# Kernel optimization log

Hardware: AMD Instinct MI355X
Metric: run time of the kernel (lower is better)

Reference implementation:

```python
import jax, jax.numpy as jnp
import numpy as np

H = 3  # heads
NEG_SLOPE = 0.2


def gat_conv(x, edge_index, W, a_src, a_dst, bias):
    # PyG GATConv: add self loops, per-head linear, edge attention, segment softmax over dst.
    N = x.shape[0]
    C = a_src.shape[1]
    loop = jnp.arange(N)
    src = jnp.concatenate([edge_index[0], loop])
    dst = jnp.concatenate([edge_index[1], loop])
    h = (x @ W).reshape(N, H, C)                      # [N,H,C]
    s_src = jnp.sum(h * a_src, axis=-1)               # [N,H]
    s_dst = jnp.sum(h * a_dst, axis=-1)               # [N,H]
    e = jax.nn.leaky_relu(s_src[src] + s_dst[dst], NEG_SLOPE)  # [E,H]
    m = jax.ops.segment_max(e, dst, num_segments=N)   # every node has a self loop -> finite
    e = jnp.exp(e - m[dst])
    denom = jax.ops.segment_sum(e, dst, num_segments=N)
    alpha = e / (denom[dst] + 1e-16)                  # [E,H]
    out = jax.ops.segment_sum(alpha[:, :, None] * h[src], dst, num_segments=N)  # [N,H,C]
    return out.reshape(N, H * C) + bias


def mlp(x, w1, b1, w2, b2):
    return jax.nn.gelu(x @ w1 + b1, approximate=False) @ w2 + b2


def glorot(k, shape):
    fan_in, fan_out = shape[-2], shape[-1]
    lim = np.sqrt(6.0 / (fan_in + fan_out))
    return jax.random.uniform(k, shape, jnp.float32, -lim, lim)


def setup_inputs() -> dict:
    key = jax.random.key(0)
    ks = jax.random.split(key, 24)
    N, E, F, C, HID = 50000, 800000, 256, 64, 128
    inp = {
        "x_st": jax.random.normal(ks[0], (N, F), jnp.float32),
        "edge_index_st": jax.random.randint(ks[1], (2, E), 0, N, jnp.int32),
        "x_sc": jax.random.normal(ks[2], (N, F), jnp.float32),
        "edge_index_sc": jax.random.randint(ks[3], (2, E), 0, N, jnp.int32),
    }
    for i, tag in enumerate(["st", "sc"]):
        o = 4 + i * 10
        inp[f"w_gat_{tag}"] = glorot(ks[o], (F, H * C))
        inp[f"a_src_{tag}"] = glorot(ks[o + 1], (H, C)) * 0.1
        inp[f"a_dst_{tag}"] = glorot(ks[o + 2], (H, C)) * 0.1
        inp[f"b_gat_{tag}"] = jnp.zeros((H * C,), jnp.float32)
        inp[f"w1_{tag}"] = glorot(ks[o + 3], (H * C, HID))
        inp[f"b1_{tag}"] = jnp.zeros((HID,), jnp.float32)
        inp[f"w2_{tag}"] = glorot(ks[o + 4], (HID, 1))
        inp[f"b2_{tag}"] = jnp.zeros((1,), jnp.float32)
    return inp


def reference(x_st, edge_index_st, x_sc, edge_index_sc,
              w_gat_st, a_src_st, a_dst_st, b_gat_st, w1_st, b1_st, w2_st, b2_st,
              w_gat_sc, a_src_sc, a_dst_sc, b_gat_sc, w1_sc, b1_sc, w2_sc, b2_sc):
    weight = 0.5
    h_st = jax.nn.elu(gat_conv(x_st, edge_index_st, w_gat_st, a_src_st, a_dst_st, b_gat_st))
    beta_st = mlp(h_st, w1_st, b1_st, w2_st, b2_st) / 100.0   # [N,1]
    z_st = x_st.T @ beta_st                                   # [F,1]
    h_sc = jax.nn.elu(gat_conv(x_sc, edge_index_sc, w_gat_sc, a_src_sc, a_dst_sc, b_gat_sc))
    beta_sc = mlp(h_sc, w1_sc, b1_sc, w2_sc, b2_sc) / 100.0
    z_sc = x_sc.T @ beta_sc
    out = jax.nn.sigmoid(z_sc + weight * z_st)
    return (out, beta_st, beta_sc)
```

## Files before the change

### kernel.cpp

```cpp
#include <hip/hip_runtime.h>
#include <math.h>

#define HEADS 3
#define CDIM 64
#define FDIM 256
#define HC 192
#define HIDDIM 128
#define NEG 0.2f

#define SCAN_BLK 256
#define SCAN_ELEMS 1024

#define ASTR2 40
#define BSTR 264
#define BSTRB 200

typedef __attribute__((ext_vector_type(8))) short short8;
typedef __attribute__((ext_vector_type(4))) float f32x4;

__device__ __forceinline__ void atomicMaxF(float* addr, float val) {
    if (val >= 0.f) atomicMax((int*)addr, __float_as_int(val));
    else            atomicMin((unsigned int*)addr, __float_as_uint(val));
}

__device__ __forceinline__ unsigned short f2bf(float f) {
    unsigned int u = __float_as_uint(f);
    u = (u + 0x7FFFu + ((u >> 16) & 1u)) >> 16;
    return (unsigned short)u;
}
__device__ __forceinline__ float bf2f(unsigned short u) {
    return __uint_as_float((unsigned int)u << 16);
}
__device__ __forceinline__ float leaky(float s) { return s >= 0.f ? s : NEG * s; }

__device__ __forceinline__ int xcd_swizzle(int orig, int nwg) {
    int q = nwg >> 3, r = nwg & 7;
    int xcd = orig & 7, idx = orig >> 3;
    return (xcd < r ? xcd * (q + 1) : r * (q + 1) + (xcd - r) * q) + idx;
}

__global__ __launch_bounds__(256) void setup(const float* __restrict__ wg_st,
                                             const float* __restrict__ wg_sc,
                                             const float* __restrict__ w1_st,
                                             const float* __restrict__ w1_sc,
                                             unsigned short* __restrict__ o0,
                                             unsigned short* __restrict__ o1,
                                             unsigned short* __restrict__ o2,
                                             unsigned short* __restrict__ o3,
                                             int* __restrict__ zero_base, int zero_ints) {
    int which = blockIdx.y;
    if (which == 4) {
        for (int i = blockIdx.x * 256 + threadIdx.x; i < zero_ints; i += gridDim.x * 256)
            zero_base[i] = 0;
        return;
    }
    const float* src = which == 0 ? wg_st : which == 1 ? wg_sc : which == 2 ? w1_st : w1_sc;
    unsigned short* dst = which == 0 ? o0 : which == 1 ? o1 : which == 2 ? o2 : o3;
    int K  = which < 2 ? FDIM : HC;
    int Nn = which < 2 ? HC : HIDDIM;
    int total = K * Nn;
    for (int idx = blockIdx.x * 256 + threadIdx.x; idx < total; idx += gridDim.x * 256) {
        int n = idx / K, k = idx - n * K;
        dst[idx] = f2bf(src[(size_t)k * Nn + n]);
    }
}

__global__ __launch_bounds__(256) void gemm_attn(const float* __restrict__ x_st,
                                                 const float* __restrict__ x_sc,
                                                 const unsigned short* __restrict__ wgT_st,
                                                 const unsigned short* __restrict__ wgT_sc,
                                                 const float* __restrict__ as_st,
                                                 const float* __restrict__ ad_st,
                                                 const float* __restrict__ as_sc,
                                                 const float* __restrict__ ad_sc,
                                                 unsigned short* __restrict__ h_bf,
                                                 float* __restrict__ ssrc,
                                                 float* __restrict__ sdst,
                                                 int M, int nrow) {
    __shared__ unsigned short As[128 * ASTR2];
    __shared__ unsigned short Bs[64 * BSTR];
    const int nwg = nrow * HEADS * 2;
    const int wgid = xcd_swizzle(blockIdx.x, nwg);
    const int tag = wgid / (nrow * HEADS);
    const int rem = wgid - tag * (nrow * HEADS);
    const int rt = rem / HEADS;
    const int head = rem - rt * HEADS;
    const float* A = tag ? x_sc : x_st;
    const unsigned short* BT = tag ? wgT_sc : wgT_st;
    const float* a_src = tag ? as_sc : as_st;
    const float* a_dst = tag ? ad_sc : ad_st;
    const int row0 = rt * 128, col0 = head * 64;
    const int tid = threadIdx.x;
    const int wv = tid >> 6, l = tid & 63;
    const int lr = l & 15, lg = l >> 4, lk = lg * 8;
    {
        int c = tid >> 2, q = tid & 3;
        const unsigned short* bp = BT + (size_t)(col0 + c) * FDIM;
        #pragma unroll
        for (int kk = q * 8; kk < FDIM; kk += 32)
            *(short8*)(Bs + c * BSTR + kk) = *(const short8*)(bp + kk);
    }
    const int arow = tid >> 1, aseg = tid & 1;
    const int gr = row0 + arow;
    f32x4 acc[2][4] = {};
    for (int ks = 0; ks < FDIM / 32; ++ks) {
        int k0 = ks * 32;
        short8 av1 = {0,0,0,0,0,0,0,0}, av2 = {0,0,0,0,0,0,0,0};
        if (gr < M) {
            const float* p = A + (size_t)gr * FDIM + k0 + aseg * 16;
            float4 x0 = *(const float4*)p;
            float4 x1 = *(const float4*)(p + 4);
            float4 x2 = *(const float4*)(p + 8);
            float4 x3 = *(const float4*)(p + 12);
            av1[0] = (short)f2bf(x0.x); av1[1] = (short)f2bf(x0.y);
            av1[2] = (short)f2bf(x0.z); av1[3] = (short)f2bf(x0.w);
            av1[4] = (short)f2bf(x1.x); av1[5] = (short)f2bf(x1.y);
            av1[6] = (short)f2bf(x1.z); av1[7] = (short)f2bf(x1.w);
            av2[0] = (short)f2bf(x2.x); av2[1] = (short)f2bf(x2.y);
            av2[2] = (short)f2bf(x2.z); av2[3] = (short)f2bf(x2.w);
            av2[4] = (short)f2bf(x3.x); av2[5] = (short)f2bf(x3.y);
            av2[6] = (short)f2bf(x3.z); av2[7] = (short)f2bf(x3.w);
        }
        *(short8*)(As + arow * ASTR2 + aseg * 16) = av1;
        *(short8*)(As + arow * ASTR2 + aseg * 16 + 8) = av2;
        __syncthreads();
        #pragma unroll
        for (int m = 0; m < 2; ++m) {
            short8 af = *(const short8*)(As + (wv * 32 + m * 16 + lr) * ASTR2 + lk);
            #pragma unroll
            for (int nb = 0; nb < 4; ++nb) {
                short8 bfm = *(const short8*)(Bs + (nb * 16 + lr) * BSTR + k0 + lk);
                acc[m][nb] = __builtin_amdgcn_mfma_f32_16x16x32_bf16(af, bfm, acc[m][nb], 0, 0, 0);
            }
        }
        __syncthreads();
    }
    const size_t tagbase = (size_t)tag * M;
    #pragma unroll
    for (int m = 0; m < 2; ++m)
        #pragma unroll
        for (int nb = 0; nb < 4; ++nb)
            #pragma unroll
            for (int r = 0; r < 4; ++r) {
                int grow = row0 + wv * 32 + m * 16 + lg * 4 + r;
                if (grow < M)
                    h_bf[(tagbase + grow) * HC + col0 + nb * 16 + lr] = f2bf(acc[m][nb][r]);
            }
    float avs[4], avd[4];
    #pragma unroll
    for (int nb = 0; nb < 4; ++nb) {
        avs[nb] = a_src[col0 + nb * 16 + lr];
        avd[nb] = a_dst[col0 + nb * 16 + lr];
    }
    #pragma unroll
    for (int m = 0; m < 2; ++m)
        #pragma unroll
        for (int r = 0; r < 4; ++r) {
            float ds = acc[m][0][r] * avs[0] + acc[m][1][r] * avs[1]
                     + acc[m][2][r] * avs[2] + acc[m][3][r] * avs[3];
            float dd = acc[m][0][r] * avd[0] + acc[m][1][r] * avd[1]
                     + acc[m][2][r] * avd[2] + acc[m][3][r] * avd[3];
            #pragma unroll
            for (int off = 8; off; off >>= 1) {
                ds += __shfl_down(ds, off);
                dd += __shfl_down(dd, off);
            }
            int grow = row0 + wv * 32 + m * 16 + lg * 4 + r;
            if (lr == 0 && grow < M) {
                ssrc[(tagbase + grow) * 3 + head] = ds;
                sdst[(tagbase + grow) * 3 + head] = dd;
            }
        }
}

__global__ __launch_bounds__(256) void prep(const int* __restrict__ ei_st,
                                            const int* __restrict__ ei_sc,
                                            int* __restrict__ deg,
                                            const float* __restrict__ ssrc,
                                            const float* __restrict__ sdst,
                                            float* __restrict__ gmax,
                                            int N, int E, int Etot) {
    if (blockIdx.y < 2) {
        int e = blockIdx.x * 256 + threadIdx.x;
        if (e >= Etot) return;
        const int* ei = blockIdx.y ? ei_sc : ei_st;
        int dst = (e < E) ? ei[E + e] : (e - E);
        atomicAdd(&deg[blockIdx.y * N + dst], 1);
        return;
    }
    if (blockIdx.x >= 32) return;
    __shared__ float red[4][12];
    float v[12];
    #pragma unroll
    for (int j = 0; j < 12; ++j) v[j] = -1e30f;
    const int stride = 32 * 256;
    for (int n = blockIdx.x * 256 + threadIdx.x; n < 2 * N; n += stride) {
        float s0 = ssrc[n * 3], s1 = ssrc[n * 3 + 1], s2 = ssrc[n * 3 + 2];
        float d0 = sdst[n * 3], d1 = sdst[n * 3 + 1], d2 = sdst[n * 3 + 2];
        if (n < N) {
            v[0] = fmaxf(v[0], s0); v[1] = fmaxf(v[1], s1); v[2] = fmaxf(v[2], s2);
            v[3] = fmaxf(v[3], d0); v[4] = fmaxf(v[4], d1); v[5] = fmaxf(v[5], d2);
        } else {
            v[6] = fmaxf(v[6], s0); v[7] = fmaxf(v[7], s1); v[8] = fmaxf(v[8], s2);
            v[9] = fmaxf(v[9], d0); v[10] = fmaxf(v[10], d1); v[11] = fmaxf(v[11], d2);
        }
    }
    #pragma unroll
    for (int j = 0; j < 12; ++j)
        #pragma unroll
        for (int off = 32; off; off >>= 1)
            v[j] = fmaxf(v[j], __shfl_down(v[j], off));
    int wave = threadIdx.x >> 6, lane = threadIdx.x & 63;
    if (lane == 0) {
        #pragma unroll
        for (int j = 0; j < 12; ++j) red[wave][j] = v[j];
    }
    __syncthreads();
    if (threadIdx.x < 12) {
        float m = fmaxf(fmaxf(red[0][threadIdx.x], red[1][threadIdx.x]),
                        fmaxf(red[2][threadIdx.x], red[3][threadIdx.x]));
        atomicMaxF(&gmax[threadIdx.x], m);
    }
}

__global__ __launch_bounds__(SCAN_BLK) void scan1(const int* __restrict__ deg,
                                                  int* __restrict__ row_ptr,
                                                  int* __restrict__ bsums, int N2) {
    __shared__ int sm[SCAN_BLK];
    int tid = threadIdx.x;
    int base = blockIdx.x * SCAN_ELEMS + tid * 4;
    int v[4];
    #pragma unroll
    for (int j = 0; j < 4; ++j) v[j] = (base + j < N2) ? deg[base + j] : 0;
    int tsum = v[0] + v[1] + v[2] + v[3];
    sm[tid] = tsum;
    __syncthreads();
    for (int off = 1; off < SCAN_BLK; off <<= 1) {
        int y = (tid >= off) ? sm[tid - off] : 0;
        __syncthreads();
        sm[tid] += y;
        __syncthreads();
    }
    int run = sm[tid] - tsum;
    #pragma unroll
    for (int j = 0; j < 4; ++j) {
        if (base + j < N2) row_ptr[base + j] = run;
        run += v[j];
    }
    if (tid == SCAN_BLK - 1) bsums[blockIdx.x] = sm[SCAN_BLK - 1];
}

__global__ __launch_bounds__(SCAN_BLK) void scan2(int* __restrict__ bsums, int nb) {
    __shared__ int sm[SCAN_BLK];
    int tid = threadIdx.x;
    int v = (tid < nb) ? bsums[tid] : 0;
    sm[tid] = v;
    __syncthreads();
    for (int off = 1; off < SCAN_BLK; off <<= 1) {
        int y = (tid >= off) ? sm[tid - off] : 0;
        __syncthreads();
        sm[tid] += y;
        __syncthreads();
    }
    if (tid < nb) bsums[tid] = sm[tid] - v;
}

__global__ __launch_bounds__(256) void scatter_p2(const int* __restrict__ ei_st,
                                                  const int* __restrict__ ei_sc,
                                                  const float* __restrict__ s_src_all,
                                                  const float* __restrict__ s_dst_all,
                                                  const float* __restrict__ gmax,
                                                  const int* __restrict__ row_ptr,
                                                  const int* __restrict__ bsums,
                                                  int* __restrict__ cursor,
                                                  f32x4* __restrict__ csr_data,
                                                  int N, int E, int Etot) {
    int e = blockIdx.x * blockDim.x + threadIdx.x;
    if (e >= Etot) return;
    const int tag = blockIdx.y;
    const int* ei = tag ? ei_sc : ei_st;
    const float* s_src = s_src_all + (size_t)tag * N * 3;
    const float* s_dst = s_dst_all + (size_t)tag * N * 3;
    const float* gm = gmax + tag * 6;
    int src, dst;
    if (e < E) { src = ei[e]; dst = ei[E + e]; } else { src = dst = e - E; }
    float M0 = leaky(gm[0] + gm[3]);
    float M1 = leaky(gm[1] + gm[4]);
    float M2 = leaky(gm[2] + gm[5]);
    float p0 = __expf(leaky(s_src[src * 3 + 0] + s_dst[dst * 3 + 0]) - M0);
    float p1 = __expf(leaky(s_src[src * 3 + 1] + s_dst[dst * 3 + 1]) - M1);
    float p2 = __expf(leaky(s_src[src * 3 + 2] + s_dst[dst * 3 + 2]) - M2);
    int g = tag * N + dst;
    int pos = row_ptr[g] + bsums[g >> 10] + atomicAdd(&cursor[g], 1);
    f32x4 val = {__int_as_float(tag * N + src), p0, p1, p2};
    csr_data[pos] = val;
}

__global__ __launch_bounds__(256) void csr_agg2(const int* __restrict__ row_ptr,
                                                const int* __restrict__ bsums,
                                                const int* __restrict__ deg,
                                                const f32x4* __restrict__ csr_data,
                                                const unsigned short* __restrict__ Hall,
                                                const float* __restrict__ bias_st,
                                                const float* __restrict__ bias_sc,
                                                unsigned short* __restrict__ og, int N) {
    int gid = blockIdx.x * blockDim.x + threadIdx.x;
    int node = gid >> 6, lane = gid & 63;
    if (node >= 2 * N) return;
    const float* bias = (node >= N) ? bias_sc : bias_st;
    int start = row_ptr[node] + bsums[node >> 10];
    int cnt = deg[node];
    float acc0 = 0.f, acc1 = 0.f, acc2 = 0.f;
    float d0 = 0.f, d1 = 0.f, d2 = 0.f;
    int i = 0;
    for (; i + 3 < cnt; i += 4) {
        f32x4 v0 = csr_data[start + i];
        f32x4 v1 = csr_data[start + i + 1];
        f32x4 v2 = csr_data[start + i + 2];
        f32x4 v3 = csr_data[start + i + 3];
        const unsigned short* r0 =
            Hall + (size_t)__builtin_amdgcn_readfirstlane(__float_as_int(v0[0])) * HC + lane;
        const unsigned short* r1 =
            Hall + (size_t)__builtin_amdgcn_readfirstlane(__float_as_int(v1[0])) * HC + lane;
        const unsigned short* r2 =
            Hall + (size_t)__builtin_amdgcn_readfirstlane(__float_as_int(v2[0])) * HC + lane;
        const unsigned short* r3 =
            Hall + (size_t)__builtin_amdgcn_readfirstlane(__float_as_int(v3[0])) * HC + lane;
        float h00 = bf2f(r0[0]), h01 = bf2f(r0[64]), h02 = bf2f(r0[128]);
        float h10 = bf2f(r1[0]), h11 = bf2f(r1[64]), h12 = bf2f(r1[128]);
        float h20 = bf2f(r2[0]), h21 = bf2f(r2[64]), h22 = bf2f(r2[128]);
        float h30 = bf2f(r3[0]), h31 = bf2f(r3[64]), h32 = bf2f(r3[128]);
        acc0 = fmaf(v0[1], h00, acc0); acc1 = fmaf(v0[2], h01, acc1); acc2 = fmaf(v0[3], h02, acc2);
        acc0 = fmaf(v1[1], h10, acc0); acc1 = fmaf(v1[2], h11, acc1); acc2 = fmaf(v1[3], h12, acc2);
        acc0 = fmaf(v2[1], h20, acc0); acc1 = fmaf(v2[2], h21, acc1); acc2 = fmaf(v2[3], h22, acc2);
        acc0 = fmaf(v3[1], h30, acc0); acc1 = fmaf(v3[2], h31, acc1); acc2 = fmaf(v3[3], h32, acc2);
        d0 += (v0[1] + v1[1]) + (v2[1] + v3[1]);
        d1 += (v0[2] + v1[2]) + (v2[2] + v3[2]);
        d2 += (v0[3] + v1[3]) + (v2[3] + v3[3]);
    }
    for (; i < cnt; ++i) {
        f32x4 v0 = csr_data[start + i];
        const unsigned short* r0 =
            Hall + (size_t)__builtin_amdgcn_readfirstlane(__float_as_int(v0[0])) * HC + lane;
        acc0 = fmaf(v0[1], bf2f(r0[0]),   acc0);
        acc1 = fmaf(v0[2], bf2f(r0[64]),  acc1);
        acc2 = fmaf(v0[3], bf2f(r0[128]), acc2);
        d0 += v0[1]; d1 += v0[2]; d2 += v0[3];
    }
    float o0 = acc0 / (d0 + 1e-16f) + bias[lane];
    float o1 = acc1 / (d1 + 1e-16f) + bias[64 + lane];
    float o2 = acc2 / (d2 + 1e-16f) + bias[128 + lane];
    o0 = o0 > 0.f ? o0 : expm1f(o0);
    o1 = o1 > 0.f ? o1 : expm1f(o1);
    o2 = o2 > 0.f ? o2 : expm1f(o2);
    unsigned short* orow = og + (size_t)node * HC + lane;
    orow[0] = f2bf(o0); orow[64] = f2bf(o1); orow[128] = f2bf(o2);
}

__global__ __launch_bounds__(256) void gemm_beta(const unsigned short* __restrict__ og_bf,
                                                 const unsigned short* __restrict__ w1T_st,
                                                 const unsigned short* __restrict__ w1T_sc,
                                                 const float* __restrict__ b1_st,
                                                 const float* __restrict__ w2_st,
                                                 const float* __restrict__ b2_st,
                                                 const float* __restrict__ b1_sc,
                                                 const float* __restrict__ w2_sc,
                                                 const float* __restrict__ b2_sc,
                                                 float* __restrict__ beta_out,
                                                 int M, int nrow) {
    __shared__ unsigned short As[128 * ASTR2];
    __shared__ unsigned short Bs[128 * BSTRB];
    const int nwg = nrow * 2;
    const int wgid = xcd_swizzle(blockIdx.x, nwg);
    const int tag = wgid / nrow;
    const int rt = wgid - tag * nrow;
    const unsigned short* A = og_bf + (size_t)tag * M * HC;
    const unsigned short* BT = tag ? w1T_sc : w1T_st;
    const float* b1 = tag ? b1_sc : b1_st;
    const float* w2 = tag ? w2_sc : w2_st;
    const float b2v = (tag ? b2_sc : b2_st)[0];
    const int row0 = rt * 128;
    const int tid = threadIdx.x;
    const int wv = tid >> 6, l = tid & 63;
    const int lr = l & 15, lg = l >> 4, lk = lg * 8;
    {
        int c = tid >> 1, half = tid & 1;
        const unsigned short* bp = BT + (size_t)c * HC;
        #pragma unroll
        for (int j = 0; j < 12; ++j) {
            int kk = half * 96 + j * 8;
            *(short8*)(Bs + c * BSTRB + kk) = *(const short8*)(bp + kk);
        }
    }
    const int arow = tid >> 1, aseg = tid & 1;
    const int gr = row0 + arow;
    f32x4 acc[2][8] = {};
    for (int ks = 0; ks < HC / 32; ++ks) {
        int k0 = ks * 32;
        short8 av1 = {0,0,0,0,0,0,0,0}, av2 = {0,0,0,0,0,0,0,0};
        if (gr < M) {
            const unsigned short* p = A + (size_t)gr * HC + k0 + aseg * 16;
            av1 = *(const short8*)p;
            av2 = *(const short8*)(p + 8);
        }
        *(short8*)(As + arow * ASTR2 + aseg * 16) = av1;
        *(short8*)(As + arow * ASTR2 + aseg * 16 + 8) = av2;
        __syncthreads();
        #pragma unroll
        for (int m = 0; m < 2; ++m) {
            short8 af = *(const short8*)(As + (wv * 32 + m * 16 + lr) * ASTR2 + lk);
            #pragma unroll
            for (int nb = 0; nb < 8; ++nb) {
                short8 bfm = *(const short8*)(Bs + (nb * 16 + lr) * BSTRB + k0 + lk);
                acc[m][nb] = __builtin_amdgcn_mfma_f32_16x16x32_bf16(af, bfm, acc[m][nb], 0, 0, 0);
            }
        }
        __syncthreads();
    }
    float b1v[8], w2v[8];
    #pragma unroll
    for (int nb = 0; nb < 8; ++nb) {
        b1v[nb] = b1[nb * 16 + lr];
        w2v[nb] = w2[nb * 16 + lr];
    }
    #pragma unroll
    for (int m = 0; m < 2; ++m)
        #pragma unroll
        for (int r = 0; r < 4; ++r) {
            float p = 0.f;
            #pragma unroll
            for (int nb = 0; nb < 8; ++nb) {
                float vx = acc[m][nb][r] + b1v[nb];
                float g = 0.5f * vx * (1.f + erff(vx * 0.70710678118654752f));
                p = fmaf(g, w2v[nb], p);
            }
            #pragma unroll
            for (int off = 8; off; off >>= 1) p += __shfl_down(p, off);
            int grow = row0 + wv * 32 + m * 16 + lg * 4 + r;
            if (lr == 0 && grow < M)
                beta_out[(size_t)tag * M + grow] = (p + b2v) * 0.01f;
        }
}

__global__ __launch_bounds__(256) void xt_beta2(const float* __restrict__ X_st,
                                                const float* __restrict__ X_sc,
                                                const float* __restrict__ beta_all,
                                                float* __restrict__ z_all, int N) {
    const int tag = blockIdx.y;
    const float* X = tag ? X_sc : X_st;
    const float* beta = beta_all + (size_t)tag * N;
    float* z = z_all + tag * FDIM;
    int f = threadIdx.x;
    int nPer = (N + gridDim.x - 1) / gridDim.x;
    int n0 = blockIdx.x * nPer;
    int n1 = min(n0 + nPer, N);
    float acc = 0.f;
    for (int n = n0; n < n1; ++n)
        acc = fmaf(X[(size_t)n * FDIM + f], beta[n], acc);
    atomicAdd(&z[f], acc);
}

__global__ void final_sigmoid(const float* __restrict__ z_all,
                              float* __restrict__ out) {
    int f = threadIdx.x;
    float v = z_all[FDIM + f] + 0.5f * z_all[f];
    out[f] = 1.f / (1.f + expf(-v));
}

extern "C" void kernel_launch(void* const* d_in, const int* in_sizes, int n_in,
                              void* d_out, int out_size, void* d_ws, size_t ws_size,
                              hipStream_t stream) {
    const float* x_st = (const float*)d_in[0];
    const int*   ei_st = (const int*)d_in[1];
    const float* x_sc = (const float*)d_in[2];
    const int*   ei_sc = (const int*)d_in[3];
    const int N = in_sizes[0] / FDIM;
    const int E = in_sizes[1] / 2;
    const int Etot = E + N;
    const int N2 = 2 * N;

    const float* wg_st   = (const float*)d_in[4];
    const float* asrc_st = (const float*)d_in[5];
    const float* adst_st = (const float*)d_in[6];
    const float* bg_st   = (const float*)d_in[7];
    const float* w1_st   = (const float*)d_in[8];
    const float* b1_st   = (const float*)d_in[9];
    const float* w2_st   = (const float*)d_in[10];
    const float* b2_st   = (const float*)d_in[11];
    const float* wg_sc   = (const float*)d_in[12];
    const float* asrc_sc = (const float*)d_in[13];
    const float* adst_sc = (const float*)d_in[14];
    const float* bg_sc   = (const float*)d_in[15];
    const float* w1_sc   = (const float*)d_in[16];
    const float* b1_sc   = (const float*)d_in[17];
    const float* w2_sc   = (const float*)d_in[18];
    const float* b2_sc   = (const float*)d_in[19];

    float* out = (float*)d_out;
    float* beta_out = out + FDIM;

    char* wp = (char*)d_ws;
    auto alloc = [&](size_t bytes) { char* r = wp; wp += (bytes + 63) & ~(size_t)63; return r; };
    const int zero_ints = 2 * N2 + 16 + 512;
    int*   degb   = (int*)alloc((size_t)zero_ints * 4);
    int*   cursor = degb + N2;
    float* gmax   = (float*)(cursor + N2);
    float* zbuf   = gmax + 16;

    unsigned short* h_bf  = (unsigned short*)alloc((size_t)N2 * HC * 2);
    unsigned short* og_bf = (unsigned short*)alloc((size_t)N2 * HC * 2);
    f32x4*          csr_data = (f32x4*)alloc((size_t)2 * Etot * 16);
    float* ssrc = (float*)alloc((size_t)N2 * 3 * 4);
    float* sdst = (float*)alloc((size_t)N2 * 3 * 4);
    int* row_ptr = (int*)alloc((size_t)N2 * 4);
    int* bsums   = (int*)alloc(SCAN_BLK * 4);
    unsigned short* wgT_st = (unsigned short*)alloc((size_t)HC * FDIM * 2);
    unsigned short* wgT_sc = (unsigned short*)alloc((size_t)HC * FDIM * 2);
    unsigned short* w1T_st = (unsigned short*)alloc((size_t)HIDDIM * HC * 2);
    unsigned short* w1T_sc = (unsigned short*)alloc((size_t)HIDDIM * HC * 2);

    const int nb_scan = (N2 + SCAN_ELEMS - 1) / SCAN_ELEMS;
    const int nrow_t = (N + 127) / 128;

    setup<<<dim3(96, 5), 256, 0, stream>>>(wg_st, wg_sc, w1_st, w1_sc,
                                           wgT_st, wgT_sc, w1T_st, w1T_sc,
                                           degb, zero_ints);

    gemm_attn<<<nrow_t * HEADS * 2, 256, 0, stream>>>(
        x_st, x_sc, wgT_st, wgT_sc, asrc_st, adst_st, asrc_sc, adst_sc,
        h_bf, ssrc, sdst, N, nrow_t);

    prep<<<dim3((Etot + 255) / 256, 3), 256, 0, stream>>>(ei_st, ei_sc, degb,
                                                          ssrc, sdst, gmax, N, E, Etot);

    scan1<<<nb_scan, SCAN_BLK, 0, stream>>>(degb, row_ptr, bsums, N2);
    scan2<<<1, SCAN_BLK, 0, stream>>>(bsums, nb_scan);

    scatter_p2<<<dim3((Etot + 255) / 256, 2), 256, 0, stream>>>(
        ei_st, ei_sc, ssrc, sdst, gmax, row_ptr, bsums, cursor, csr_data, N, E, Etot);

    csr_agg2<<<(N2 + 3) / 4, 256, 0, stream>>>(row_ptr, bsums, degb, csr_data, h_bf,
                                               bg_st, bg_sc, og_bf, N);

    gemm_beta<<<nrow_t * 2, 256, 0, stream>>>(og_bf, w1T_st, w1T_sc,
                                              b1_st, w2_st, b2_st,
                                              b1_sc, w2_sc, b2_sc, beta_out, N, nrow_t);

    xt_beta2<<<dim3(512, 2), 256, 0, stream>>>(x_st, x_sc, beta_out, zbuf, N);

    final_sigmoid<<<1, FDIM, 0, stream>>>(zbuf, out);
}
```

Baseline: 385.1 us.

## Compute all heads per GAT GEMM block and fold degree counting into setup

The attention GEMM now uses 512-thread blocks that each compute all 192 output columns for a 128-row tile, so every x row is read and converted to bf16 once instead of once per head. The per-head attention dot products are summed through shared-memory atomics. Degree counting moves into the setup kernel, zeroing switches to hipMemsetAsync, and the scan runs before the GEMM. The global max becomes its own small kernel, and xt_beta2 launches with fewer blocks. In exchange the block needs far more LDS (192 rows of B), which lowers occupancy, and the shared-atomic reduction adds some overhead.

```diff
diff --git a/kernel.cpp b/kernel.cpp
--- a/kernel.cpp
+++ b/kernel.cpp
@@ -47,11 +47,17 @@
                                              unsigned short* __restrict__ o1,
                                              unsigned short* __restrict__ o2,
                                              unsigned short* __restrict__ o3,
-                                             int* __restrict__ zero_base, int zero_ints) {
+                                             const int* __restrict__ ei_st,
+                                             const int* __restrict__ ei_sc,
+                                             int* __restrict__ deg,
+                                             int N, int E, int Etot) {
     int which = blockIdx.y;
-    if (which == 4) {
-        for (int i = blockIdx.x * 256 + threadIdx.x; i < zero_ints; i += gridDim.x * 256)
-            zero_base[i] = 0;
+    if (which >= 4) {
+        int e = blockIdx.x * 256 + threadIdx.x;
+        if (e >= Etot) return;
+        const int* ei = (which == 5) ? ei_sc : ei_st;
+        int dst = (e < E) ? ei[E + e] : (e - E);
+        atomicAdd(&deg[(which - 4) * N + dst], 1);
         return;
     }
     const float* src = which == 0 ? wg_st : which == 1 ? wg_sc : which == 2 ? w1_st : w1_sc;
@@ -65,71 +71,61 @@
     }
 }
 
-__global__ __launch_bounds__(256) void gemm_attn(const float* __restrict__ x_st,
-                                                 const float* __restrict__ x_sc,
-                                                 const unsigned short* __restrict__ wgT_st,
-                                                 const unsigned short* __restrict__ wgT_sc,
-                                                 const float* __restrict__ as_st,
-                                                 const float* __restrict__ ad_st,
-                                                 const float* __restrict__ as_sc,
-                                                 const float* __restrict__ ad_sc,
-                                                 unsigned short* __restrict__ h_bf,
-                                                 float* __restrict__ ssrc,
-                                                 float* __restrict__ sdst,
-                                                 int M, int nrow) {
+__global__ __launch_bounds__(512) void gemm_attn3(const float* __restrict__ x_st,
+                                                  const float* __restrict__ x_sc,
+                                                  const unsigned short* __restrict__ wgT_st,
+                                                  const unsigned short* __restrict__ wgT_sc,
+                                                  const float* __restrict__ as_st,
+                                                  const float* __restrict__ ad_st,
+                                                  const float* __restrict__ as_sc,
+                                                  const float* __restrict__ ad_sc,
+                                                  unsigned short* __restrict__ h_bf,
+                                                  float* __restrict__ ssrc,
+                                                  float* __restrict__ sdst,
+                                                  int M, int nrow) {
     __shared__ unsigned short As[128 * ASTR2];
-    __shared__ unsigned short Bs[64 * BSTR];
-    const int nwg = nrow * HEADS * 2;
+    __shared__ unsigned short Bs[192 * BSTR];
+    __shared__ float sred[128][3][2];
+    const int nwg = nrow * 2;
     const int wgid = xcd_swizzle(blockIdx.x, nwg);
-    const int tag = wgid / (nrow * HEADS);
-    const int rem = wgid - tag * (nrow * HEADS);
-    const int rt = rem / HEADS;
-    const int head = rem - rt * HEADS;
+    const int tag = wgid / nrow;
+    const int rt = wgid - tag * nrow;
     const float* A = tag ? x_sc : x_st;
     const unsigned short* BT = tag ? wgT_sc : wgT_st;
     const float* a_src = tag ? as_sc : as_st;
     const float* a_dst = tag ? ad_sc : ad_st;
-    const int row0 = rt * 128, col0 = head * 64;
+    const int row0 = rt * 128;
     const int tid = threadIdx.x;
     const int wv = tid >> 6, l = tid & 63;
+    const int wrow = wv >> 2, wcol = wv & 3;
     const int lr = l & 15, lg = l >> 4, lk = lg * 8;
-    {
-        int c = tid >> 2, q = tid & 3;
-        const unsigned short* bp = BT + (size_t)(col0 + c) * FDIM;
-        #pragma unroll
-        for (int kk = q * 8; kk < FDIM; kk += 32)
-            *(short8*)(Bs + c * BSTR + kk) = *(const short8*)(bp + kk);
-    }
-    const int arow = tid >> 1, aseg = tid & 1;
+    for (int li = tid; li < 192 * 32; li += 512) {
+        int c = li >> 5, seg = li & 31;
+        *(short8*)(Bs + c * BSTR + seg * 8) = *(const short8*)(BT + (size_t)c * FDIM + seg * 8);
+    }
+    const int arow = tid >> 2, aseg = tid & 3;
     const int gr = row0 + arow;
-    f32x4 acc[2][4] = {};
+    f32x4 acc[4][3] = {};
     for (int ks = 0; ks < FDIM / 32; ++ks) {
         int k0 = ks * 32;
-        short8 av1 = {0,0,0,0,0,0,0,0}, av2 = {0,0,0,0,0,0,0,0};
+        short8 av = {0,0,0,0,0,0,0,0};
         if (gr < M) {
-            const float* p = A + (size_t)gr * FDIM + k0 + aseg * 16;
+            const float* p = A + (size_t)gr * FDIM + k0 + aseg * 8;
             float4 x0 = *(const float4*)p;
             float4 x1 = *(const float4*)(p + 4);
-            float4 x2 = *(const float4*)(p + 8);
-            float4 x3 = *(const float4*)(p + 12);
-            av1[0] = (short)f2bf(x0.x); av1[1] = (short)f2bf(x0.y);
-            av1[2] = (short)f2bf(x0.z); av1[3] = (short)f2bf(x0.w);
-            av1[4] = (short)f2bf(x1.x); av1[5] = (short)f2bf(x1.y);
-            av1[6] = (short)f2bf(x1.z); av1[7] = (short)f2bf(x1.w);
-            av2[0] = (short)f2bf(x2.x); av2[1] = (short)f2bf(x2.y);
-            av2[2] = (short)f2bf(x2.z); av2[3] = (short)f2bf(x2.w);
-            av2[4] = (short)f2bf(x3.x); av2[5] = (short)f2bf(x3.y);
-            av2[6] = (short)f2bf(x3.z); av2[7] = (short)f2bf(x3.w);
-        }
-        *(short8*)(As + arow * ASTR2 + aseg * 16) = av1;
-        *(short8*)(As + arow * ASTR2 + aseg * 16 + 8) = av2;
-        __syncthreads();
-        #pragma unroll
-        for (int m = 0; m < 2; ++m) {
-            short8 af = *(const short8*)(As + (wv * 32 + m * 16 + lr) * ASTR2 + lk);
+            av[0] = (short)f2bf(x0.x); av[1] = (short)f2bf(x0.y);
+            av[2] = (short)f2bf(x0.z); av[3] = (short)f2bf(x0.w);
+            av[4] = (short)f2bf(x1.x); av[5] = (short)f2bf(x1.y);
+            av[6] = (short)f2bf(x1.z); av[7] = (short)f2bf(x1.w);
+        }
+        *(short8*)(As + arow * ASTR2 + aseg * 8) = av;
+        __syncthreads();
+        #pragma unroll
+        for (int m = 0; m < 4; ++m) {
+            short8 af = *(const short8*)(As + (wrow * 64 + m * 16 + lr) * ASTR2 + lk);
             #pragma unroll
-            for (int nb = 0; nb < 4; ++nb) {
-                short8 bfm = *(const short8*)(Bs + (nb * 16 + lr) * BSTR + k0 + lk);
+            for (int nb = 0; nb < 3; ++nb) {
+                short8 bfm = *(const short8*)(Bs + (wcol * 48 + nb * 16 + lr) * BSTR + k0 + lk);
                 acc[m][nb] = __builtin_amdgcn_mfma_f32_16x16x32_bf16(af, bfm, acc[m][nb], 0, 0, 0);
             }
         }
@@ -137,58 +133,55 @@
     }
     const size_t tagbase = (size_t)tag * M;
     #pragma unroll
-    for (int m = 0; m < 2; ++m)
-        #pragma unroll
-        for (int nb = 0; nb < 4; ++nb)
+    for (int m = 0; m < 4; ++m)
+        #pragma unroll
+        for (int nb = 0; nb < 3; ++nb)
             #pragma unroll
             for (int r = 0; r < 4; ++r) {
-                int grow = row0 + wv * 32 + m * 16 + lg * 4 + r;
+                int grow = row0 + wrow * 64 + m * 16 + lg * 4 + r;
                 if (grow < M)
-                    h_bf[(tagbase + grow) * HC + col0 + nb * 16 + lr] = f2bf(acc[m][nb][r]);
+                    h_bf[(tagbase + grow) * HC + wcol * 48 + nb * 16 + lr] = f2bf(acc[m][nb][r]);
             }
-    float avs[4], avd[4];
-    #pragma unroll
-    for (int nb = 0; nb < 4; ++nb) {
-        avs[nb] = a_src[col0 + nb * 16 + lr];
-        avd[nb] = a_dst[col0 + nb * 16 + lr];
-    }
-    #pragma unroll
-    for (int m = 0; m < 2; ++m)
-        #pragma unroll
-        for (int r = 0; r < 4; ++r) {
-            float ds = acc[m][0][r] * avs[0] + acc[m][1][r] * avs[1]
-                     + acc[m][2][r] * avs[2] + acc[m][3][r] * avs[3];
-            float dd = acc[m][0][r] * avd[0] + acc[m][1][r] * avd[1]
-                     + acc[m][2][r] * avd[2] + acc[m][3][r] * avd[3];
+    for (int i = tid; i < 128 * 3 * 2; i += 512) ((float*)sred)[i] = 0.f;
+    __syncthreads();
+    #pragma unroll
+    for (int m = 0; m < 4; ++m)
+        #pragma unroll
+        for (int nb = 0; nb < 3; ++nb) {
+            int colb = wcol * 48 + nb * 16;
+            int hd = colb >> 6;
+            float avs = a_src[colb + lr];
+            float avd = a_dst[colb + lr];
             #pragma unroll
-            for (int off = 8; off; off >>= 1) {
-                ds += __shfl_down(ds, off);
-                dd += __shfl_down(dd, off);
+            for (int r = 0; r < 4; ++r) {
+                float ds = acc[m][nb][r] * avs;
+                float dd = acc[m][nb][r] * avd;
+                #pragma unroll
+                for (int off = 8; off; off >>= 1) {
+                    ds += __shfl_down(ds, off);
+                    dd += __shfl_down(dd, off);
+                }
+                if (lr == 0) {
+                    int lrow = wrow * 64 + m * 16 + lg * 4 + r;
+                    atomicAdd(&sred[lrow][hd][0], ds);
+                    atomicAdd(&sred[lrow][hd][1], dd);
+                }
             }
-            int grow = row0 + wv * 32 + m * 16 + lg * 4 + r;
-            if (lr == 0 && grow < M) {
-                ssrc[(tagbase + grow) * 3 + head] = ds;
-                sdst[(tagbase + grow) * 3 + head] = dd;
-            }
-        }
-}
-
-__global__ __launch_bounds__(256) void prep(const int* __restrict__ ei_st,
-                                            const int* __restrict__ ei_sc,
-                                            int* __restrict__ deg,
-                                            const float* __restrict__ ssrc,
-                                            const float* __restrict__ sdst,
-                                            float* __restrict__ gmax,
-                                            int N, int E, int Etot) {
-    if (blockIdx.y < 2) {
-        int e = blockIdx.x * 256 + threadIdx.x;
-        if (e >= Etot) return;
-        const int* ei = blockIdx.y ? ei_sc : ei_st;
-        int dst = (e < E) ? ei[E + e] : (e - E);
-        atomicAdd(&deg[blockIdx.y * N + dst], 1);
-        return;
-    }
-    if (blockIdx.x >= 32) return;
+        }
+    __syncthreads();
+    for (int i = tid; i < 128 * 3; i += 512) {
+        int lrow = i / 3, hd = i - lrow * 3;
+        int grow = row0 + lrow;
+        if (grow < M) {
+            ssrc[(tagbase + grow) * 3 + hd] = sred[lrow][hd][0];
+            sdst[(tagbase + grow) * 3 + hd] = sred[lrow][hd][1];
+        }
+    }
+}
+
+__global__ __launch_bounds__(256) void gmax32(const float* __restrict__ ssrc,
+                                              const float* __restrict__ sdst,
+                                              float* __restrict__ gmax, int N) {
     __shared__ float red[4][12];
     float v[12];
     #pragma unroll
@@ -521,22 +514,24 @@
 
     const int nb_scan = (N2 + SCAN_ELEMS - 1) / SCAN_ELEMS;
     const int nrow_t = (N + 127) / 128;
-
-    setup<<<dim3(96, 5), 256, 0, stream>>>(wg_st, wg_sc, w1_st, w1_sc,
-                                           wgT_st, wgT_sc, w1T_st, w1T_sc,
-                                           degb, zero_ints);
-
-    gemm_attn<<<nrow_t * HEADS * 2, 256, 0, stream>>>(
+    const int nblk_e = (Etot + 255) / 256;
+
+    hipMemsetAsync(degb, 0, (size_t)zero_ints * 4, stream);
+
+    setup<<<dim3(nblk_e, 6), 256, 0, stream>>>(wg_st, wg_sc, w1_st, w1_sc,
+                                               wgT_st, wgT_sc, w1T_st, w1T_sc,
+                                               ei_st, ei_sc, degb, N, E, Etot);
+
+    scan1<<<nb_scan, SCAN_BLK, 0, stream>>>(degb, row_ptr, bsums, N2);
+    scan2<<<1, SCAN_BLK, 0, stream>>>(bsums, nb_scan);
+
+    gemm_attn3<<<nrow_t * 2, 512, 0, stream>>>(
         x_st, x_sc, wgT_st, wgT_sc, asrc_st, adst_st, asrc_sc, adst_sc,
         h_bf, ssrc, sdst, N, nrow_t);
 
-    prep<<<dim3((Etot + 255) / 256, 3), 256, 0, stream>>>(ei_st, ei_sc, degb,
-                                                          ssrc, sdst, gmax, N, E, Etot);
-
-    scan1<<<nb_scan, SCAN_BLK, 0, stream>>>(degb, row_ptr, bsums, N2);
-    scan2<<<1, SCAN_BLK, 0, stream>>>(bsums, nb_scan);
-
-    scatter_p2<<<dim3((Etot + 255) / 256, 2), 256, 0, stream>>>(
+    gmax32<<<32, 256, 0, stream>>>(ssrc, sdst, gmax, N);
+
+    scatter_p2<<<dim3(nblk_e, 2), 256, 0, stream>>>(
         ei_st, ei_sc, ssrc, sdst, gmax, row_ptr, bsums, cursor, csr_data, N, E, Etot);
 
     csr_agg2<<<(N2 + 3) / 4, 256, 0, stream>>>(row_ptr, bsums, degb, csr_data, h_bf,
@@ -546,7 +541,7 @@
                                               b1_st, w2_st, b2_st,
                                               b1_sc, w2_sc, b2_sc, beta_out, N, nrow_t);
 
-    xt_beta2<<<dim3(512, 2), 256, 0, stream>>>(x_st, x_sc, beta_out, zbuf, N);
+    xt_beta2<<<dim3(160, 2), 256, 0, stream>>>(x_st, x_sc, beta_out, zbuf, N);
 
     final_sigmoid<<<1, FDIM, 0, stream>>>(zbuf, out);
 }
```

Measured after the change: 491.6 us. 27.7% more time.
